# Kernel optimization log

Measured on AMD Instinct MI355X. Metric: run time of the kernel, lower is better.

Reference implementation:

```python
import jax, jax.numpy as jnp
import numpy as np

L = 4        # num_hidden_layers
D = 1024     # dmodel (== inputsize)
FF = 4096    # dff
H = 16       # num_heads
DH = D // H  # head dim
B, S = 2, 2048
EPS = 1e-6


def _layer_norm(x, g, b):
    m = jnp.mean(x, axis=-1, keepdims=True)
    v = jnp.mean(jnp.square(x - m), axis=-1, keepdims=True)
    return (x - m) * jax.lax.rsqrt(v + EPS) * g + b


def setup_inputs() -> dict:
    key = jax.random.key(0)
    ks = jax.random.split(key, 16)
    sd = 0.02
    inp = {
        "hidden_states": jax.random.normal(ks[0], (B, S, D), jnp.float32),
        # stacked per-layer params (weights stored [in, out])
        "Wq": jax.random.normal(ks[1], (L, D, D), jnp.float32) * sd,
        "bq": jnp.zeros((L, D), jnp.float32),
        "Wk": jax.random.normal(ks[2], (L, D, D), jnp.float32) * sd,
        "bk": jnp.zeros((L, D), jnp.float32),
        "Wv": jax.random.normal(ks[3], (L, D, D), jnp.float32) * sd,
        "bv": jnp.zeros((L, D), jnp.float32),
        "Wp": jax.random.normal(ks[4], (L, D, D), jnp.float32) * sd,
        "bp": jnp.zeros((L, D), jnp.float32),
        "ln1_g": jnp.ones((L, D), jnp.float32),
        "ln1_b": jnp.zeros((L, D), jnp.float32),
        "W1": jax.random.normal(ks[5], (L, D, FF), jnp.float32) * sd,
        "b1": jnp.zeros((L, FF), jnp.float32),
        "W2": jax.random.normal(ks[6], (L, FF, D), jnp.float32) * sd,
        "b2": jnp.zeros((L, D), jnp.float32),
        "ln2_g": jnp.ones((L, D), jnp.float32),
        "ln2_b": jnp.zeros((L, D), jnp.float32),
    }
    return inp


def reference(hidden_states, Wq, bq, Wk, bk, Wv, bv, Wp, bp, ln1_g, ln1_b,
              W1, b1, W2, b2, ln2_g, ln2_b):
    x = hidden_states
    scale = 1.0 / jnp.sqrt(jnp.asarray(DH, x.dtype))
    for l in range(L):
        # --- AttentionIn ---
        q = (x @ Wq[l] + bq[l]).reshape(B, S, H, DH)
        k = (x @ Wk[l] + bk[l]).reshape(B, S, H, DH)
        v = (x @ Wv[l] + bv[l]).reshape(B, S, H, DH)
        scores = jnp.einsum('bqhd,bkhd->bhqk', q, k) * scale
        probs = jax.nn.softmax(scores, axis=-1)
        ctx = jnp.einsum('bhqk,bkhd->bqhd', probs, v).reshape(B, S, D)
        ctx = ctx @ Wp[l] + bp[l]
        x = _layer_norm(ctx + x, ln1_g[l], ln1_b[l])
        # --- AttentionOutput (FFN with residual + LN); dropout=0 ---
        h = jax.nn.relu(x @ W1[l] + b1[l]) @ W2[l] + b2[l]
        x = _layer_norm(h + x, ln2_g[l], ln2_b[l])
    return x
```

## Files before the change

### kernel.cpp

```cpp
#include <hip/hip_runtime.h>

#define D_  1024
#define FF_ 4096
#define H_  16
#define DH_ 64
#define B_  2
#define S_  2048
#define M_  4096

typedef __attribute__((ext_vector_type(8))) __bf16 bf16x8;
typedef __attribute__((ext_vector_type(4))) short short4v;
typedef __attribute__((ext_vector_type(4))) float floatx4;

typedef __attribute__((address_space(1))) unsigned int as1_uint;
typedef __attribute__((address_space(3))) unsigned int as3_uint;

__device__ __forceinline__ unsigned short f2bf(float f) {
    unsigned u = __float_as_uint(f);
    u += 0x7FFFu + ((u >> 16) & 1u);
    return (unsigned short)(u >> 16);
}

__device__ __forceinline__ int packbf(float a, float b) {
    return (int)((__float_as_uint(a) >> 16) | (__float_as_uint(b) & 0xFFFF0000u));
}

__device__ __forceinline__ void gl_lds16(const void* g, void* l) {
    __builtin_amdgcn_global_load_lds((as1_uint*)(unsigned long long)g,
                                     (as3_uint*)l, 16, 0, 0);
}

__global__ __launch_bounds__(256) void transpose_cvt(
    const float* __restrict__ src, unsigned short* __restrict__ dst, int K, int N)
{
    __shared__ float tile[32][33];
    const int tx = threadIdx.x, ty = threadIdx.y;
    const int n0 = blockIdx.x * 32, k0 = blockIdx.y * 32;
#pragma unroll
    for (int i = 0; i < 32; i += 8)
        tile[ty + i][tx] = src[(size_t)(k0 + ty + i) * N + n0 + tx];
    __syncthreads();
#pragma unroll
    for (int i = 0; i < 32; i += 8)
        dst[(size_t)(n0 + ty + i) * K + k0 + tx] = f2bf(tile[tx][ty + i]);
}

__global__ __launch_bounds__(256) void transpose_v(
    const unsigned short* __restrict__ V, unsigned short* __restrict__ VT)
{
    __shared__ unsigned short t[64][72];
    const int bh = blockIdx.y, s0 = blockIdx.x * 64;
    const int tid = threadIdx.x;
#pragma unroll
    for (int i = 0; i < 2; i++) {
        int u = tid + i * 256;
        int s = u >> 3, dc = u & 7;
        uint4 v = *(const uint4*)(V + ((size_t)bh * S_ + s0 + s) * DH_ + dc * 8);
        *(uint4*)&t[s][dc * 8] = v;
    }
    __syncthreads();
    const int dh = tid >> 2, sc = (tid & 3) * 16;
    unsigned v[16];
#pragma unroll
    for (int j = 0; j < 16; j++) v[j] = t[sc + j][dh];
    uint4 o0, o1;
    o0.x = v[0] | (v[1] << 16);  o0.y = v[2] | (v[3] << 16);
    o0.z = v[4] | (v[5] << 16);  o0.w = v[6] | (v[7] << 16);
    o1.x = v[8] | (v[9] << 16);  o1.y = v[10] | (v[11] << 16);
    o1.z = v[12] | (v[13] << 16); o1.w = v[14] | (v[15] << 16);
    unsigned short* dst = VT + ((size_t)bh * DH_ + dh) * S_ + s0 + sc;
    *(uint4*)dst = o0;
    *(uint4*)(dst + 8) = o1;
}

__global__ __launch_bounds__(256) void cvt_x0(
    const float* __restrict__ in, float* __restrict__ xf, unsigned short* __restrict__ xh)
{
    int i = blockIdx.x * 256 + threadIdx.x;
    float4 v = ((const float4*)in)[i];
    ((float4*)xf)[i] = v;
    uint2 h;
    h.x = (unsigned)f2bf(v.x) | ((unsigned)f2bf(v.y) << 16);
    h.y = (unsigned)f2bf(v.z) | ((unsigned)f2bf(v.w) << 16);
    ((uint2*)xh)[i] = h;
}

template <int EPI, int KSPLIT>
__global__ __launch_bounds__(256) void gemm128(
    const unsigned short* __restrict__ A, const unsigned short* __restrict__ BT,
    int M, int N, int K,
    const float* __restrict__ b0, const float* __restrict__ b1, const float* __restrict__ b2,
    float* __restrict__ outF, unsigned short* __restrict__ outH,
    unsigned short* __restrict__ qO, unsigned short* __restrict__ kO, unsigned short* __restrict__ vO)
{
    __shared__ __align__(16) unsigned short As[128 * 64];
    __shared__ __align__(16) unsigned short Bs[128 * 64];

    const int tid = threadIdx.x;
    const int m0 = blockIdx.y * 128, n0 = blockIdx.x * 128;
    const int kchunk = K / KSPLIT;
    const int kbase = (KSPLIT > 1) ? (int)blockIdx.z * kchunk : 0;
    const int lane = tid & 63, wv = tid >> 6;
    const int wm = wv & 1, wn = wv >> 1;
    const int cl = lane & 15, quad = lane >> 4;

    const int srow = tid >> 3, sslot = tid & 7;
    const int schk = sslot ^ (srow & 7);
    const unsigned short* gA = A  + (size_t)(m0 + srow) * K + kbase + schk * 8;
    const unsigned short* gB = BT + (size_t)(n0 + srow) * K + kbase + schk * 8;

    floatx4 acc[4][4];
#pragma unroll
    for (int i = 0; i < 4; i++)
#pragma unroll
        for (int j = 0; j < 4; j++) acc[i][j] = (floatx4){0.f, 0.f, 0.f, 0.f};

    for (int kt = 0; kt < kchunk; kt += 64) {
#pragma unroll
        for (int i = 0; i < 4; i++) {
            gl_lds16(gA + (size_t)(32 * i) * K + kt, &As[(size_t)(tid + 256 * i) * 8]);
            gl_lds16(gB + (size_t)(32 * i) * K + kt, &Bs[(size_t)(tid + 256 * i) * 8]);
        }
        __syncthreads();

        bf16x8 av[4][2], bv[4][2];
#pragma unroll
        for (int mi = 0; mi < 4; mi++) {
            const int row = wm * 64 + mi * 16 + cl;
#pragma unroll
            for (int ks = 0; ks < 2; ks++)
                av[mi][ks] = *(const bf16x8*)&As[row * 64 + (((ks * 4 + quad) ^ (cl & 7)) * 8)];
        }
#pragma unroll
        for (int ni = 0; ni < 4; ni++) {
            const int row = wn * 64 + ni * 16 + cl;
#pragma unroll
            for (int ks = 0; ks < 2; ks++)
                bv[ni][ks] = *(const bf16x8*)&Bs[row * 64 + (((ks * 4 + quad) ^ (cl & 7)) * 8)];
        }
#pragma unroll
        for (int mi = 0; mi < 4; mi++)
#pragma unroll
            for (int ni = 0; ni < 4; ni++) {
                acc[mi][ni] = __builtin_amdgcn_mfma_f32_16x16x32_bf16(
                    av[mi][0], bv[ni][0], acc[mi][ni], 0, 0, 0);
                acc[mi][ni] = __builtin_amdgcn_mfma_f32_16x16x32_bf16(
                    av[mi][1], bv[ni][1], acc[mi][ni], 0, 0, 0);
            }
        __syncthreads();
    }

    float* outFz = (EPI == 0) ? outF + (size_t)blockIdx.z * M * N : outF;
#pragma unroll
    for (int mi = 0; mi < 4; mi++) {
#pragma unroll
        for (int ni = 0; ni < 4; ni++) {
            const int c = n0 + wn * 64 + ni * 16 + cl;
#pragma unroll
            for (int r = 0; r < 4; r++) {
                const int rr = m0 + wm * 64 + mi * 16 + quad * 4 + r;
                float v = acc[mi][ni][r];
                if (EPI == 0) {
                    outFz[(size_t)rr * N + c] = v;
                } else if (EPI == 1) {
                    float t = v + b0[c];
                    outH[(size_t)rr * N + c] = f2bf(t > 0.f ? t : 0.f);
                } else {
                    const int kind = c >> 10, cc = c & 1023;
                    const float* bp = (kind == 0) ? b0 : (kind == 1) ? b1 : b2;
                    float t = v + bp[cc];
                    if (kind == 0) t *= 0.18033688f;
                    const int h = cc >> 6, dh = cc & 63;
                    const int bb = rr >> 11, s = rr & 2047;
                    unsigned short* dst = (kind == 0) ? qO : (kind == 1) ? kO : vO;
                    dst[((size_t)(bb * H_ + h) * S_ + s) * DH_ + dh] = f2bf(t);
                }
            }
        }
    }
}

__global__ __launch_bounds__(256) void attn_kernel(
    const unsigned short* __restrict__ Qg, const unsigned short* __restrict__ Kg,
    const unsigned short* __restrict__ VTg, unsigned short* __restrict__ ctx)
{
    __shared__ __align__(16) unsigned short Ks[64 * 64];
    __shared__ __align__(16) unsigned short Vs[64 * 64];

    const int tid = threadIdx.x, lane = tid & 63, wv = tid >> 6;
    const int cl = lane & 15, quad = lane >> 4;

    const int lin = blockIdx.x;
    const int idx = lin >> 3;
    const int bh  = (lin & 7) * 4 + (idx & 3);
    const int qt  = idx >> 2;
    const int qrow = qt * 64 + wv * 16 + cl;
    const size_t bhS = (size_t)bh * S_;

    bf16x8 aq[2];
#pragma unroll
    for (int ks = 0; ks < 2; ks++)
        aq[ks] = *(const bf16x8*)(Qg + (bhS + qrow) * DH_ + ks * 32 + quad * 8);

    floatx4 O[4];
#pragma unroll
    for (int i = 0; i < 4; i++) O[i] = (floatx4){0.f, 0.f, 0.f, 0.f};
    float l_cur = 0.f;

    const int g0 = tid, g1 = tid + 256;
    const int r_0 = g0 >> 3, c_0 = (g0 & 7) ^ (r_0 & 7);
    const int r_1 = g1 >> 3, c_1 = (g1 & 7) ^ (r_1 & 7);
    const unsigned short* kp0 = Kg + (bhS + r_0) * DH_ + c_0 * 8;
    const unsigned short* kp1 = Kg + (bhS + r_1) * DH_ + c_1 * 8;
    const unsigned short* vp0 = VTg + ((size_t)bh * DH_ + r_0) * S_ + c_0 * 8;
    const unsigned short* vp1 = VTg + ((size_t)bh * DH_ + r_1) * S_ + c_1 * 8;
    unsigned short* lk0 = &Ks[(size_t)g0 * 8];
    unsigned short* lk1 = &Ks[(size_t)g1 * 8];
    unsigned short* lv0 = &Vs[(size_t)g0 * 8];
    unsigned short* lv1 = &Vs[(size_t)g1 * 8];

    const unsigned short* krd0[4];
    const unsigned short* krd1[4];
    const unsigned short* vrd[4][4];
#pragma unroll
    for (int mi = 0; mi < 4; mi++) {
        const int row = mi * 16 + cl;
        krd0[mi] = &Ks[(row * 8 + (quad       ^ (cl & 7))) * 8];
        krd1[mi] = &Ks[(row * 8 + ((4 + quad) ^ (cl & 7))) * 8];
#pragma unroll
        for (int c16 = 0; c16 < 4; c16++) {
            const int slot = (c16 * 2 + (quad >> 1)) ^ (cl & 7);
            vrd[c16][mi] = &Vs[(row * 8 + slot) * 8 + (quad & 1) * 4];
        }
    }

    for (int k0 = 0; k0 < S_; k0 += 64) {
        __syncthreads();
        gl_lds16(kp0 + (size_t)k0 * DH_, lk0);
        gl_lds16(kp1 + (size_t)k0 * DH_, lk1);
        gl_lds16(vp0 + k0, lv0);
        gl_lds16(vp1 + k0, lv1);
        __syncthreads();

        floatx4 sc[4];
#pragma unroll
        for (int mi = 0; mi < 4; mi++) {
            bf16x8 kf0 = *(const bf16x8*)krd0[mi];
            bf16x8 kf1 = *(const bf16x8*)krd1[mi];
            floatx4 z = (floatx4){0.f, 0.f, 0.f, 0.f};
            z = __builtin_amdgcn_mfma_f32_16x16x32_bf16(kf0, aq[0], z, 0, 0, 0);
            sc[mi] = __builtin_amdgcn_mfma_f32_16x16x32_bf16(kf1, aq[1], z, 0, 0, 0);
        }

        int pk[4][2];
#pragma unroll
        for (int mi = 0; mi < 4; mi++) {
            float p0 = __builtin_amdgcn_exp2f(sc[mi][0]);
            float p1 = __builtin_amdgcn_exp2f(sc[mi][1]);
            float p2 = __builtin_amdgcn_exp2f(sc[mi][2]);
            float p3 = __builtin_amdgcn_exp2f(sc[mi][3]);
            l_cur += (p0 + p1) + (p2 + p3);
            pk[mi][0] = packbf(p0, p1);
            pk[mi][1] = packbf(p2, p3);
        }

#pragma unroll
        for (int c16 = 0; c16 < 4; c16++) {
            union { int i[2]; short4v s; } pb;
            pb.i[0] = pk[c16][0];
            pb.i[1] = pk[c16][1];
#pragma unroll
            for (int mi2 = 0; mi2 < 4; mi2++) {
                short4v va = *(const short4v*)vrd[c16][mi2];
                O[mi2] = __builtin_amdgcn_mfma_f32_16x16x16bf16_1k(va, pb.s, O[mi2], 0, 0, 0);
            }
        }
    }

    l_cur += __shfl_xor(l_cur, 16);
    l_cur += __shfl_xor(l_cur, 32);

    const float invl = 1.f / l_cur;
    const int b = bh >> 4, h = bh & 15;
    unsigned short* cp = ctx + ((size_t)(b * S_ + qrow)) * D_ + h * DH_ + quad * 4;
#pragma unroll
    for (int mi2 = 0; mi2 < 4; mi2++) {
        unsigned short w[4];
#pragma unroll
        for (int r = 0; r < 4; r++) w[r] = f2bf(O[mi2][r] * invl);
        unsigned o0 = (unsigned)w[0] | ((unsigned)w[1] << 16);
        unsigned o1 = (unsigned)w[2] | ((unsigned)w[3] << 16);
        uint2 ov; ov.x = o0; ov.y = o1;
        *(uint2*)(cp + mi2 * 16) = ov;
    }
}

template <int NP>
__global__ __launch_bounds__(256) void ln_kernel(
    const float* __restrict__ t, const float* __restrict__ bias,
    const float* __restrict__ xr,
    const float* __restrict__ g, const float* __restrict__ b,
    float* __restrict__ xf, unsigned short* __restrict__ xh, float* __restrict__ extra)
{
    const int row = blockIdx.x, tid = threadIdx.x;
    float4 a = ((const float4*)(t + (size_t)row * D_))[tid];
#pragma unroll
    for (int p = 1; p < NP; p++) {
        const float4 ap = ((const float4*)(t + (size_t)p * M_ * D_ + (size_t)row * D_))[tid];
        a.x += ap.x; a.y += ap.y; a.z += ap.z; a.w += ap.w;
    }
    const float4 bs = ((const float4*)bias)[tid];
    const float4 c = ((const float4*)(xr + (size_t)row * D_))[tid];
    float4 y;
    y.x = a.x + bs.x + c.x; y.y = a.y + bs.y + c.y;
    y.z = a.z + bs.z + c.z; y.w = a.w + bs.w + c.w;
    float s  = y.x + y.y + y.z + y.w;
    float sq = y.x * y.x + y.y * y.y + y.z * y.z + y.w * y.w;
#pragma unroll
    for (int off = 1; off < 64; off <<= 1) {
        s  += __shfl_xor(s, off);
        sq += __shfl_xor(sq, off);
    }
    __shared__ float red[8];
    const int wv = tid >> 6, lane = tid & 63;
    if (lane == 0) { red[wv] = s; red[4 + wv] = sq; }
    __syncthreads();
    s  = red[0] + red[1] + red[2] + red[3];
    sq = red[4] + red[5] + red[6] + red[7];
    const float mean = s * (1.f / D_);
    const float var  = sq * (1.f / D_) - mean * mean;
    const float ri   = rsqrtf(var + 1e-6f);
    const float4 gg = ((const float4*)g)[tid];
    const float4 bb = ((const float4*)b)[tid];
    float4 o;
    o.x = (y.x - mean) * ri * gg.x + bb.x;
    o.y = (y.y - mean) * ri * gg.y + bb.y;
    o.z = (y.z - mean) * ri * gg.z + bb.z;
    o.w = (y.w - mean) * ri * gg.w + bb.w;
    ((float4*)(xf + (size_t)row * D_))[tid] = o;
    uint2 h;
    h.x = (unsigned)f2bf(o.x) | ((unsigned)f2bf(o.y) << 16);
    h.y = (unsigned)f2bf(o.z) | ((unsigned)f2bf(o.w) << 16);
    ((uint2*)(xh + (size_t)row * D_))[tid] = h;
    if (extra) ((float4*)(extra + (size_t)row * D_))[tid] = o;
}

extern "C" void kernel_launch(void* const* d_in, const int* in_sizes, int n_in,
                              void* d_out, int out_size, void* d_ws, size_t ws_size,
                              hipStream_t stream)
{
    const float* hs  = (const float*)d_in[0];
    const float* Wq  = (const float*)d_in[1];
    const float* bq  = (const float*)d_in[2];
    const float* Wk  = (const float*)d_in[3];
    const float* bk  = (const float*)d_in[4];
    const float* Wv  = (const float*)d_in[5];
    const float* bv  = (const float*)d_in[6];
    const float* Wp  = (const float*)d_in[7];
    const float* bp  = (const float*)d_in[8];
    const float* g1  = (const float*)d_in[9];
    const float* be1 = (const float*)d_in[10];
    const float* W1  = (const float*)d_in[11];
    const float* b1  = (const float*)d_in[12];
    const float* W2  = (const float*)d_in[13];
    const float* b2  = (const float*)d_in[14];
    const float* g2  = (const float*)d_in[15];
    const float* be2 = (const float*)d_in[16];

    char* w = (char*)d_ws;
    auto alloc = [&](size_t bytes) { char* p = w; w += (bytes + 255) & ~(size_t)255; return p; };
    unsigned short* wqkvT = (unsigned short*)alloc(3072ull * 1024 * 2);
    unsigned short* wpT   = (unsigned short*)alloc(1024ull * 1024 * 2);
    unsigned short* w1T   = (unsigned short*)alloc(4096ull * 1024 * 2);
    unsigned short* w2T   = (unsigned short*)alloc(1024ull * 4096 * 2);
    float*          xf    = (float*)alloc(4096ull * 1024 * 4);
    unsigned short* xh    = (unsigned short*)alloc(4096ull * 1024 * 2);
    unsigned short* qb_   = (unsigned short*)alloc(4096ull * 1024 * 2);
    unsigned short* kb_   = (unsigned short*)alloc(4096ull * 1024 * 2);
    unsigned short* vb_   = (unsigned short*)alloc(4096ull * 1024 * 2);
    unsigned short* ctx   = (unsigned short*)alloc(4096ull * 1024 * 2);
    float*          part  = (float*)alloc(2ull * 4096 * 1024 * 4);
    unsigned short* hh    = (unsigned short*)alloc(4096ull * 4096 * 2);
    unsigned short* vtb   = hh;

    const dim3 blk(256);
    const dim3 tb(32, 8);

    cvt_x0<<<4096, blk, 0, stream>>>(hs, xf, xh);

    for (int l = 0; l < 4; l++) {
        transpose_cvt<<<dim3(32, 32),  tb, 0, stream>>>(Wq + (size_t)l * D_ * D_,  wqkvT,                 D_, D_);
        transpose_cvt<<<dim3(32, 32),  tb, 0, stream>>>(Wk + (size_t)l * D_ * D_,  wqkvT + 1024 * 1024,   D_, D_);
        transpose_cvt<<<dim3(32, 32),  tb, 0, stream>>>(Wv + (size_t)l * D_ * D_,  wqkvT + 2 * 1024 * 1024, D_, D_);
        transpose_cvt<<<dim3(32, 32),  tb, 0, stream>>>(Wp + (size_t)l * D_ * D_,  wpT, D_, D_);
        transpose_cvt<<<dim3(128, 32), tb, 0, stream>>>(W1 + (size_t)l * D_ * FF_, w1T, D_, FF_);
        transpose_cvt<<<dim3(32, 128), tb, 0, stream>>>(W2 + (size_t)l * FF_ * D_, w2T, FF_, D_);

        gemm128<2, 1><<<dim3(24, 32), blk, 0, stream>>>(xh, wqkvT, M_, 3 * D_, D_,
            bq + l * D_, bk + l * D_, bv + l * D_,
            nullptr, nullptr, qb_, kb_, vb_);

        transpose_v<<<dim3(32, 32), blk, 0, stream>>>(vb_, vtb);

        attn_kernel<<<1024, blk, 0, stream>>>(qb_, kb_, vtb, ctx);

        gemm128<0, 2><<<dim3(8, 32, 2), blk, 0, stream>>>(ctx, wpT, M_, D_, D_,
            nullptr, nullptr, nullptr, part, nullptr, nullptr, nullptr, nullptr);

        ln_kernel<2><<<4096, blk, 0, stream>>>(part, bp + l * D_, xf,
            g1 + l * D_, be1 + l * D_, xf, xh, nullptr);

        gemm128<1, 1><<<dim3(32, 32), blk, 0, stream>>>(xh, w1T, M_, FF_, D_,
            b1 + l * FF_, nullptr, nullptr, nullptr, hh, nullptr, nullptr, nullptr);

        gemm128<0, 2><<<dim3(8, 32, 2), blk, 0, stream>>>(hh, w2T, M_, D_, FF_,
            nullptr, nullptr, nullptr, part, nullptr, nullptr, nullptr, nullptr);

        ln_kernel<2><<<4096, blk, 0, stream>>>(part, b2 + l * D_, xf,
            g2 + l * D_, be2 + l * D_, xf, xh,
            (l == 3) ? (float*)d_out : nullptr);
    }
}
```

Before: 1.195 ms.

## Batch weight transposes, double-buffer attention K/V, and split-K 4 for FFN down GEMM

Merges the six per-layer weight transpose/convert launches into one batched kernel that uses a segment table. The attention kernel now double-buffers its K/V LDS tiles, so the next tile's global-to-LDS load is issued before computing on the current one, and one barrier per iteration is dropped. The W2 GEMM goes from split-K 2 to split-K 4, with the extra partials stored in the Q buffer and summed in the LN kernel. These trade more LDS use and more partial-sum traffic for fewer launches, better latency hiding and more GEMM parallelism.

```diff
diff --git a/kernel.cpp b/kernel.cpp
--- a/kernel.cpp
+++ b/kernel.cpp
@@ -30,19 +30,26 @@
                                      (as3_uint*)l, 16, 0, 0);
 }
 
-__global__ __launch_bounds__(256) void transpose_cvt(
-    const float* __restrict__ src, unsigned short* __restrict__ dst, int K, int N)
+struct TDesc { const float* src; unsigned short* dst; int K; int N; int ntx; };
+struct TPack { TDesc d[6]; int cum[7]; };
+
+__global__ __launch_bounds__(256) void transpose_cvt_batch(TPack p)
 {
     __shared__ float tile[32][33];
+    int bid = blockIdx.x;
+    int seg = 0;
+    while (bid >= p.cum[seg + 1]) ++seg;
+    const TDesc d = p.d[seg];
+    const int t = bid - p.cum[seg];
+    const int n0 = (t % d.ntx) * 32, k0 = (t / d.ntx) * 32;
     const int tx = threadIdx.x, ty = threadIdx.y;
-    const int n0 = blockIdx.x * 32, k0 = blockIdx.y * 32;
 #pragma unroll
     for (int i = 0; i < 32; i += 8)
-        tile[ty + i][tx] = src[(size_t)(k0 + ty + i) * N + n0 + tx];
+        tile[ty + i][tx] = d.src[(size_t)(k0 + ty + i) * d.N + n0 + tx];
     __syncthreads();
 #pragma unroll
     for (int i = 0; i < 32; i += 8)
-        dst[(size_t)(n0 + ty + i) * K + k0 + tx] = f2bf(tile[tx][ty + i]);
+        d.dst[(size_t)(n0 + ty + i) * d.K + k0 + tx] = f2bf(tile[tx][ty + i]);
 }
 
 __global__ __launch_bounds__(256) void transpose_v(
@@ -90,7 +97,7 @@
     const unsigned short* __restrict__ A, const unsigned short* __restrict__ BT,
     int M, int N, int K,
     const float* __restrict__ b0, const float* __restrict__ b1, const float* __restrict__ b2,
-    float* __restrict__ outF, unsigned short* __restrict__ outH,
+    float* __restrict__ outF, float* __restrict__ outF2, unsigned short* __restrict__ outH,
     unsigned short* __restrict__ qO, unsigned short* __restrict__ kO, unsigned short* __restrict__ vO)
 {
     __shared__ __align__(16) unsigned short As[128 * 64];
@@ -150,7 +157,11 @@
         __syncthreads();
     }
 
-    float* outFz = (EPI == 0) ? outF + (size_t)blockIdx.z * M * N : outF;
+    float* outFz = nullptr;
+    if (EPI == 0) {
+        const int z = (KSPLIT > 1) ? (int)blockIdx.z : 0;
+        outFz = ((z < 2) ? outF : outF2) + (size_t)(z & 1) * M * N;
+    }
 #pragma unroll
     for (int mi = 0; mi < 4; mi++) {
 #pragma unroll
@@ -184,8 +195,8 @@
     const unsigned short* __restrict__ Qg, const unsigned short* __restrict__ Kg,
     const unsigned short* __restrict__ VTg, unsigned short* __restrict__ ctx)
 {
-    __shared__ __align__(16) unsigned short Ks[64 * 64];
-    __shared__ __align__(16) unsigned short Vs[64 * 64];
+    __shared__ __align__(16) unsigned short Ks[2][64 * 64];
+    __shared__ __align__(16) unsigned short Vs[2][64 * 64];
 
     const int tid = threadIdx.x, lane = tid & 63, wv = tid >> 6;
     const int cl = lane & 15, quad = lane >> 4;
@@ -214,39 +225,43 @@
     const unsigned short* kp1 = Kg + (bhS + r_1) * DH_ + c_1 * 8;
     const unsigned short* vp0 = VTg + ((size_t)bh * DH_ + r_0) * S_ + c_0 * 8;
     const unsigned short* vp1 = VTg + ((size_t)bh * DH_ + r_1) * S_ + c_1 * 8;
-    unsigned short* lk0 = &Ks[(size_t)g0 * 8];
-    unsigned short* lk1 = &Ks[(size_t)g1 * 8];
-    unsigned short* lv0 = &Vs[(size_t)g0 * 8];
-    unsigned short* lv1 = &Vs[(size_t)g1 * 8];
-
-    const unsigned short* krd0[4];
-    const unsigned short* krd1[4];
-    const unsigned short* vrd[4][4];
+
+    int koff0[4], koff1[4], voff[4][4];
 #pragma unroll
     for (int mi = 0; mi < 4; mi++) {
         const int row = mi * 16 + cl;
-        krd0[mi] = &Ks[(row * 8 + (quad       ^ (cl & 7))) * 8];
-        krd1[mi] = &Ks[(row * 8 + ((4 + quad) ^ (cl & 7))) * 8];
+        koff0[mi] = (row * 8 + (quad       ^ (cl & 7))) * 8;
+        koff1[mi] = (row * 8 + ((4 + quad) ^ (cl & 7))) * 8;
 #pragma unroll
         for (int c16 = 0; c16 < 4; c16++) {
             const int slot = (c16 * 2 + (quad >> 1)) ^ (cl & 7);
-            vrd[c16][mi] = &Vs[(row * 8 + slot) * 8 + (quad & 1) * 4];
-        }
-    }
-
-    for (int k0 = 0; k0 < S_; k0 += 64) {
+            voff[c16][mi] = (row * 8 + slot) * 8 + (quad & 1) * 4;
+        }
+    }
+
+    gl_lds16(kp0, &Ks[0][(size_t)g0 * 8]);
+    gl_lds16(kp1, &Ks[0][(size_t)g1 * 8]);
+    gl_lds16(vp0, &Vs[0][(size_t)g0 * 8]);
+    gl_lds16(vp1, &Vs[0][(size_t)g1 * 8]);
+
+    for (int t = 0; t < S_ / 64; t++) {
         __syncthreads();
-        gl_lds16(kp0 + (size_t)k0 * DH_, lk0);
-        gl_lds16(kp1 + (size_t)k0 * DH_, lk1);
-        gl_lds16(vp0 + k0, lv0);
-        gl_lds16(vp1 + k0, lv1);
-        __syncthreads();
+        if (t < S_ / 64 - 1) {
+            const int k0n = (t + 1) * 64;
+            const int bn = (t + 1) & 1;
+            gl_lds16(kp0 + (size_t)k0n * DH_, &Ks[bn][(size_t)g0 * 8]);
+            gl_lds16(kp1 + (size_t)k0n * DH_, &Ks[bn][(size_t)g1 * 8]);
+            gl_lds16(vp0 + k0n, &Vs[bn][(size_t)g0 * 8]);
+            gl_lds16(vp1 + k0n, &Vs[bn][(size_t)g1 * 8]);
+        }
+        const unsigned short* Kb = Ks[t & 1];
+        const unsigned short* Vb = Vs[t & 1];
 
         floatx4 sc[4];
 #pragma unroll
         for (int mi = 0; mi < 4; mi++) {
-            bf16x8 kf0 = *(const bf16x8*)krd0[mi];
-            bf16x8 kf1 = *(const bf16x8*)krd1[mi];
+            bf16x8 kf0 = *(const bf16x8*)&Kb[koff0[mi]];
+            bf16x8 kf1 = *(const bf16x8*)&Kb[koff1[mi]];
             floatx4 z = (floatx4){0.f, 0.f, 0.f, 0.f};
             z = __builtin_amdgcn_mfma_f32_16x16x32_bf16(kf0, aq[0], z, 0, 0, 0);
             sc[mi] = __builtin_amdgcn_mfma_f32_16x16x32_bf16(kf1, aq[1], z, 0, 0, 0);
@@ -271,7 +286,7 @@
             pb.i[1] = pk[c16][1];
 #pragma unroll
             for (int mi2 = 0; mi2 < 4; mi2++) {
-                short4v va = *(const short4v*)vrd[c16][mi2];
+                short4v va = *(const short4v*)&Vb[voff[c16][mi2]];
                 O[mi2] = __builtin_amdgcn_mfma_f32_16x16x16bf16_1k(va, pb.s, O[mi2], 0, 0, 0);
             }
         }
@@ -297,8 +312,8 @@
 
 template <int NP>
 __global__ __launch_bounds__(256) void ln_kernel(
-    const float* __restrict__ t, const float* __restrict__ bias,
-    const float* __restrict__ xr,
+    const float* __restrict__ t, const float* __restrict__ t2,
+    const float* __restrict__ bias, const float* __restrict__ xr,
     const float* __restrict__ g, const float* __restrict__ b,
     float* __restrict__ xf, unsigned short* __restrict__ xh, float* __restrict__ extra)
 {
@@ -306,7 +321,8 @@
     float4 a = ((const float4*)(t + (size_t)row * D_))[tid];
 #pragma unroll
     for (int p = 1; p < NP; p++) {
-        const float4 ap = ((const float4*)(t + (size_t)p * M_ * D_ + (size_t)row * D_))[tid];
+        const float* src = ((p < 2) ? t : t2) + (size_t)(p & 1) * M_ * D_;
+        const float4 ap = ((const float4*)(src + (size_t)row * D_))[tid];
         a.x += ap.x; a.y += ap.y; a.z += ap.z; a.w += ap.w;
     }
     const float4 bs = ((const float4*)bias)[tid];
@@ -382,6 +398,7 @@
     float*          part  = (float*)alloc(2ull * 4096 * 1024 * 4);
     unsigned short* hh    = (unsigned short*)alloc(4096ull * 4096 * 2);
     unsigned short* vtb   = hh;
+    float*          part2 = (float*)qb_;
 
     const dim3 blk(256);
     const dim3 tb(32, 8);
@@ -389,34 +406,38 @@
     cvt_x0<<<4096, blk, 0, stream>>>(hs, xf, xh);
 
     for (int l = 0; l < 4; l++) {
-        transpose_cvt<<<dim3(32, 32),  tb, 0, stream>>>(Wq + (size_t)l * D_ * D_,  wqkvT,                 D_, D_);
-        transpose_cvt<<<dim3(32, 32),  tb, 0, stream>>>(Wk + (size_t)l * D_ * D_,  wqkvT + 1024 * 1024,   D_, D_);
-        transpose_cvt<<<dim3(32, 32),  tb, 0, stream>>>(Wv + (size_t)l * D_ * D_,  wqkvT + 2 * 1024 * 1024, D_, D_);
-        transpose_cvt<<<dim3(32, 32),  tb, 0, stream>>>(Wp + (size_t)l * D_ * D_,  wpT, D_, D_);
-        transpose_cvt<<<dim3(128, 32), tb, 0, stream>>>(W1 + (size_t)l * D_ * FF_, w1T, D_, FF_);
-        transpose_cvt<<<dim3(32, 128), tb, 0, stream>>>(W2 + (size_t)l * FF_ * D_, w2T, FF_, D_);
+        TPack tp;
+        tp.d[0] = { Wq + (size_t)l * D_ * D_,  wqkvT,                   D_,  D_,  32 };
+        tp.d[1] = { Wk + (size_t)l * D_ * D_,  wqkvT + 1024 * 1024,     D_,  D_,  32 };
+        tp.d[2] = { Wv + (size_t)l * D_ * D_,  wqkvT + 2 * 1024 * 1024, D_,  D_,  32 };
+        tp.d[3] = { Wp + (size_t)l * D_ * D_,  wpT,                     D_,  D_,  32 };
+        tp.d[4] = { W1 + (size_t)l * D_ * FF_, w1T,                     D_,  FF_, 128 };
+        tp.d[5] = { W2 + (size_t)l * FF_ * D_, w2T,                     FF_, D_,  32 };
+        tp.cum[0] = 0;    tp.cum[1] = 1024; tp.cum[2] = 2048; tp.cum[3] = 3072;
+        tp.cum[4] = 4096; tp.cum[5] = 8192; tp.cum[6] = 12288;
+        transpose_cvt_batch<<<12288, tb, 0, stream>>>(tp);
 
         gemm128<2, 1><<<dim3(24, 32), blk, 0, stream>>>(xh, wqkvT, M_, 3 * D_, D_,
             bq + l * D_, bk + l * D_, bv + l * D_,
-            nullptr, nullptr, qb_, kb_, vb_);
+            nullptr, nullptr, nullptr, qb_, kb_, vb_);
 
         transpose_v<<<dim3(32, 32), blk, 0, stream>>>(vb_, vtb);
 
         attn_kernel<<<1024, blk, 0, stream>>>(qb_, kb_, vtb, ctx);
 
         gemm128<0, 2><<<dim3(8, 32, 2), blk, 0, stream>>>(ctx, wpT, M_, D_, D_,
-            nullptr, nullptr, nullptr, part, nullptr, nullptr, nullptr, nullptr);
-
-        ln_kernel<2><<<4096, blk, 0, stream>>>(part, bp + l * D_, xf,
+            nullptr, nullptr, nullptr, part, part, nullptr, nullptr, nullptr, nullptr);
+
+        ln_kernel<2><<<4096, blk, 0, stream>>>(part, part, bp + l * D_, xf,
             g1 + l * D_, be1 + l * D_, xf, xh, nullptr);
 
         gemm128<1, 1><<<dim3(32, 32), blk, 0, stream>>>(xh, w1T, M_, FF_, D_,
-            b1 + l * FF_, nullptr, nullptr, nullptr, hh, nullptr, nullptr, nullptr);
-
-        gemm128<0, 2><<<dim3(8, 32, 2), blk, 0, stream>>>(hh, w2T, M_, D_, FF_,
-            nullptr, nullptr, nullptr, part, nullptr, nullptr, nullptr, nullptr);
-
-        ln_kernel<2><<<4096, blk, 0, stream>>>(part, b2 + l * D_, xf,
+            b1 + l * FF_, nullptr, nullptr, nullptr, nullptr, hh, nullptr, nullptr, nullptr);
+
+        gemm128<0, 4><<<dim3(8, 32, 4), blk, 0, stream>>>(hh, w2T, M_, D_, FF_,
+            nullptr, nullptr, nullptr, part, part2, nullptr, nullptr, nullptr, nullptr);
+
+        ln_kernel<4><<<4096, blk, 0, stream>>>(part, part2, b2 + l * D_, xf,
             g2 + l * D_, be2 + l * D_, xf, xh,
             (l == 3) ? (float*)d_out : nullptr);
     }
```

Result: slower. 1.240 ms (+3.8%).
